# Kernel tuning notes

Measured on AMD Instinct MI355X. Metric: run time of the kernel, lower is better.

## Reference

```python
import jax, jax.numpy as jnp
import numpy as np

PAD_ID = 0


def setup_inputs() -> dict:
    key = jax.random.key(0)
    ks = jax.random.split(key, 14)
    B, S, T = 64, 128, 32
    E = H = 512
    V = 32000
    s = 0.02
    return {
        "trg_tokens": jax.random.randint(ks[0], (B, T), 0, V),
        "src_tokens": jax.random.randint(ks[1], (B, S), 0, V),
        "encoder_out": jax.random.normal(ks[2], (S, B, 2 * H), jnp.float32),
        "hidden": jax.random.normal(ks[3], (B, H), jnp.float32),
        "embed_w": jax.random.normal(ks[4], (V, E), jnp.float32) * s,
        "attn_W": jax.random.normal(ks[5], (H, 2 * H + H), jnp.float32) * s,
        "attn_b": jnp.zeros((H,), jnp.float32),
        "v": jax.random.uniform(ks[6], (H,), jnp.float32),
        "W_ih": jax.random.normal(ks[7], (3 * H, 2 * H + E), jnp.float32) * s,
        "W_hh": jax.random.normal(ks[8], (3 * H, H), jnp.float32) * s,
        "b_ih": jnp.zeros((3 * H,), jnp.float32),
        "b_hh": jnp.zeros((3 * H,), jnp.float32),
        "out_W": jax.random.normal(ks[9], (V, 2 * H + H + E), jnp.float32) * s,
        "out_b": jnp.zeros((V,), jnp.float32),
    }


def reference(trg_tokens, src_tokens, encoder_out, hidden, embed_w, attn_W,
              attn_b, v, W_ih, W_hh, b_ih, b_hh, out_W, out_b):
    # trg_tokens: [B, T], src_tokens: [B, S] (transposed inside, as in torch)
    B, T = trg_tokens.shape
    S = src_tokens.shape[1]
    H = hidden.shape[1]
    V = out_W.shape[0]

    # Embedding with padding_idx -> zero row at PAD_ID
    emb = embed_w.at[PAD_ID].set(0.0)
    mask = (src_tokens != PAD_ID)              # [B, S]
    enc_bt = jnp.transpose(encoder_out, (1, 0, 2))  # [B, S, 2H]
    trg = trg_tokens.T                          # [T, B]

    def step(h, tok):
        x = emb[tok]                            # [B, E]
        # Bahdanau attention
        hrep = jnp.broadcast_to(h[:, None, :], (B, S, H))
        feat = jnp.concatenate([hrep, enc_bt], axis=2)      # [B, S, H+2H]
        energy = jnp.tanh(feat @ attn_W.T + attn_b)          # [B, S, H]
        scores = jnp.einsum('bsd,d->bs', energy, v)          # [B, S]
        scores = jnp.where(mask, scores, -jnp.inf)
        attn = jax.nn.softmax(scores, axis=1)                # [B, S]
        weighted = jnp.einsum('bs,bsd->bd', attn, enc_bt)    # [B, 2H]
        # GRU cell (torch gate order: r, z, n)
        rnn_in = jnp.concatenate([x, weighted], axis=1)      # [B, E+2H]
        gi = rnn_in @ W_ih.T + b_ih                          # [B, 3H]
        gh = h @ W_hh.T + b_hh                               # [B, 3H]
        i_r, i_z, i_n = jnp.split(gi, 3, axis=1)
        h_r, h_z, h_n = jnp.split(gh, 3, axis=1)
        r = jax.nn.sigmoid(i_r + h_r)
        z = jax.nn.sigmoid(i_z + h_z)
        n = jnp.tanh(i_n + r * h_n)
        h_new = (1.0 - z) * n + z * h                        # [B, H]
        # Output projection over cat(output, weighted, x)
        out_feat = jnp.concatenate([h_new, weighted, x], axis=1)  # [B, 2H+H+E]
        logits = out_feat @ out_W.T + out_b                  # [B, V]
        return h_new, logits

    # Teacher forcing ratio = 1.0: inputs are trg[0:T-1]; outputs[0] stays zero
    _, logits_seq = jax.lax.scan(step, hidden, trg[:T - 1])  # [T-1, B, V]
    outputs = jnp.concatenate(
        [jnp.zeros((1, B, V), logits_seq.dtype), logits_seq], axis=0)
    return outputs
```

## Files before the change

kernel.cpp:

```cpp
#include <hip/hip_runtime.h>

typedef __attribute__((ext_vector_type(4))) float f32x4;
typedef __attribute__((ext_vector_type(2))) float f32x2;
typedef __attribute__((ext_vector_type(8))) short s16x8;
typedef __attribute__((ext_vector_type(4))) short s16x4;

#define B_ 64
#define S_ 128
#define T_ 32
#define H_ 512
#define V_ 32000
#define NTILES 2000

#define SY_TILE 32
#define SY_SLOT 64

__device__ __forceinline__ unsigned short f2bf(float f) {
  union { float f; unsigned u; } x; x.f = f;
  unsigned r = x.u + 0x7FFFu + ((x.u >> 16) & 1u);
  return (unsigned short)(r >> 16);
}
__device__ __forceinline__ float bf2f(unsigned short u) {
  union { unsigned u; float f; } x; x.u = ((unsigned)u) << 16; return x.f;
}
__device__ __forceinline__ float fast_tanh(float x) {
  float e = __expf(2.0f * x);
  return 1.0f - 2.0f / (e + 1.0f);
}
__device__ __forceinline__ float fast_sig(float x) {
  return 1.0f / (1.0f + __expf(-x));
}
__device__ __forceinline__ void gload16(const void* g, void* l) {
  __builtin_amdgcn_global_load_lds(
      (const __attribute__((address_space(1))) void*)g,
      (__attribute__((address_space(3))) void*)l, 16, 0, 0);
}
__device__ __forceinline__ void gload16nt(const void* g, void* l) {
  __builtin_amdgcn_global_load_lds(
      (const __attribute__((address_space(1))) void*)g,
      (__attribute__((address_space(3))) void*)l, 16, 0, 2);
}

__device__ __forceinline__ unsigned ald(const unsigned* p) {
  return __hip_atomic_load(p, __ATOMIC_RELAXED, __HIP_MEMORY_SCOPE_AGENT);
}
__device__ __forceinline__ void ast(unsigned* p, unsigned v) {
  __hip_atomic_store(p, v, __ATOMIC_RELAXED, __HIP_MEMORY_SCOPE_AGENT);
}
__device__ __forceinline__ void astf(float* p, float v) {
  union { unsigned u; float f; } x; x.f = v; ast((unsigned*)p, x.u);
}

__device__ __forceinline__ void phase_sync(unsigned* sync, int bid,
                                           unsigned st_ph, int nmask,
                                           unsigned wt_ph) {
  __syncthreads();
  if (threadIdx.x == 0)
    __hip_atomic_store(&sync[SY_SLOT + bid], st_ph, __ATOMIC_RELAXED,
                       __HIP_MEMORY_SCOPE_AGENT);
  if (threadIdx.x < 64) {
    const unsigned* p = &sync[SY_SLOT + (threadIdx.x & nmask)];
    while (ald(p) < wt_ph) __builtin_amdgcn_s_sleep(1);
  }
  __syncthreads();
}

template <int OUTBF>
__global__ __launch_bounds__(256) void big_gemm_k(
    const unsigned short* __restrict__ A, int lda,
    const unsigned short* __restrict__ W, const float* __restrict__ bias,
    void* __restrict__ Cv, int Mv, int N, int K) {
  __shared__ unsigned short As[128 * 32];
  __shared__ unsigned short Bs[128 * 32];
  const int t = threadIdx.x;
  const int wave = t >> 6, lane = t & 63;
  const int m0 = blockIdx.x * 128, n0 = blockIdx.y * 128;
  const int wm = (wave & 1) * 64, wn = (wave >> 1) * 64;
  const int fr = lane & 15, fq = lane >> 4;

  f32x4 acc[4][4];
#pragma unroll
  for (int i = 0; i < 4; ++i)
#pragma unroll
    for (int j = 0; j < 4; ++j) acc[i][j] = (f32x4){0.f, 0.f, 0.f, 0.f};

  const int g = (((lane & 3) ^ ((lane >> 3) & 3))) * 8;
  const size_t a_g0 = (size_t)(m0 + wave * 32 + (lane >> 2)) * lda + g;
  const size_t b_g0 = (size_t)(n0 + wave * 32 + (lane >> 2)) * K + g;
  unsigned short* As_w = As + wave * 1024;
  unsigned short* Bs_w = Bs + wave * 1024;
  const int sl = (fq ^ ((fr >> 1) & 3)) * 8;

  for (int kk = 0; kk < K; kk += 32) {
    gload16(A + a_g0 + kk, As_w);
    gload16(A + a_g0 + (size_t)16 * lda + kk, As_w + 512);
    gload16(W + b_g0 + kk, Bs_w);
    gload16(W + b_g0 + (size_t)16 * K + kk, Bs_w + 512);
    __syncthreads();
    s16x8 af[4], bfr[4];
#pragma unroll
    for (int f = 0; f < 4; ++f) {
      af[f] = *(const s16x8*)(As + (wm + f * 16 + fr) * 32 + sl);
      bfr[f] = *(const s16x8*)(Bs + (wn + f * 16 + fr) * 32 + sl);
    }
#pragma unroll
    for (int fm = 0; fm < 4; ++fm)
#pragma unroll
      for (int fn = 0; fn < 4; ++fn)
        acc[fm][fn] = __builtin_amdgcn_mfma_f32_16x16x32_bf16(af[fm], bfr[fn],
                                                              acc[fm][fn], 0, 0, 0);
    __syncthreads();
  }

#pragma unroll
  for (int fn = 0; fn < 4; ++fn) {
    int col = n0 + wn + fn * 16 + fr;
    float bv = bias[col];
#pragma unroll
    for (int fm = 0; fm < 4; ++fm) {
      int rb = m0 + wm + fm * 16 + fq * 4;
#pragma unroll
      for (int i = 0; i < 4; ++i) {
        int r = rb + i;
        if (r < Mv) {
          if (OUTBF)
            ((unsigned short*)Cv)[(size_t)r * N + col] = f2bf(acc[fm][fn][i] + bv);
          else
            ((float*)Cv)[(size_t)r * N + col] = acc[fm][fn][i] + bv;
        }
      }
    }
  }
}

__global__ __launch_bounds__(512) void fused_k(
    float* __restrict__ h, unsigned short* __restrict__ hbf_step,
    float* __restrict__ hgh_step, const unsigned short* __restrict__ Wcomb,
    const unsigned short* __restrict__ encp_bf,
    const unsigned short* __restrict__ enc_bf, const float* __restrict__ v,
    const int* __restrict__ src_tok, const unsigned short* __restrict__ Ww,
    const unsigned short* __restrict__ gix, const float* __restrict__ b_hh,
    unsigned short* __restrict__ Abf, const unsigned short* __restrict__ outW,
    const float* __restrict__ out_b, float* __restrict__ out,
    unsigned* __restrict__ sync) {
  __shared__ __align__(16) char smem[65536];
  const int t = threadIdx.x;
  const int lane = t & 63, w = t >> 6;
  const int fr = lane & 15, fq = lane >> 4;

  if (blockIdx.x < 64) {
    unsigned short* A0 = (unsigned short*)smem;
    unsigned short* A1 = (unsigned short*)(smem + 9216);
    unsigned short* W0 = (unsigned short*)(smem + 18432);
    unsigned short* W1 = (unsigned short*)(smem + 25344);
    unsigned short* Wp1 = (unsigned short*)(smem + 32256);
    float* gsm = (float*)smem;
    float* sc = (float*)(smem + 12288);
    const int j = blockIdx.x;
    const int ar = t >> 3, ak = (t & 7) * 8;
    const int p1_n0 = j * 32;
    const int rowt_p1 = w & 3, colt_p1 = w >> 2;

#pragma unroll
    for (int c = 0; c < 4; ++c) {
      int id = t * 4 + c;
      int r = id >> 6, cc = id & 63;
      s16x8 wv = *(const s16x8*)(Wcomb + (size_t)(p1_n0 + r) * 512 + cc * 8);
      *(s16x8*)(Wp1 + r * 520 + cc * 8) = wv;
    }

    const int rowt = (w < 4) ? w : (w - 4);
    const int wgate = ar >> 4, wdr = ar & 15;
    const int d0 = j * 16;
    const unsigned short* wwrow =
        Ww + (size_t)(wgate * 512 + d0 + wdr) * 1024 + ak;
    s16x8 pwreg[16];
    if (j < 32 && t < 384) {
#pragma unroll
      for (int p = 0; p < 16; ++p) pwreg[p] = *(const s16x8*)(wwrow + p * 64);
    }
    __syncthreads();

    for (int step = 0; step < 31; ++step) {
      const unsigned short* hbfS = hbf_step + (size_t)step * 64 * 512;
      unsigned short* hbfS1 = hbf_step + (size_t)(step + 1) * 64 * 512;
      float* hghS = hgh_step + (size_t)step * 64 * 2048;
      const unsigned ph = 3u * step;

      {
        s16x8 pa[8];
#pragma unroll
        for (int p = 0; p < 8; ++p)
          pa[p] = *(const s16x8*)(hbfS + ar * 512 + p * 64 + ak);
        *(s16x8*)(A0 + ar * 72 + ak) = pa[0];
        __syncthreads();
        f32x4 acc = {0.f, 0.f, 0.f, 0.f};
#pragma unroll
        for (int it = 0; it < 8; ++it) {
          unsigned short* bufR = (it & 1) ? A1 : A0;
          unsigned short* bufW = (it & 1) ? A0 : A1;
          s16x8 a0 = *(const s16x8*)(bufR + (rowt_p1 * 16 + fr) * 72 + fq * 8);
          s16x8 a1 =
              *(const s16x8*)(bufR + (rowt_p1 * 16 + fr) * 72 + 32 + fq * 8);
          if (it < 7) *(s16x8*)(bufW + ar * 72 + ak) = pa[it + 1];
          s16x8 b0 =
              *(const s16x8*)(Wp1 + (colt_p1 * 16 + fr) * 520 + it * 64 + fq * 8);
          s16x8 b1 = *(const s16x8*)(Wp1 + (colt_p1 * 16 + fr) * 520 + it * 64 +
                                     32 + fq * 8);
          acc = __builtin_amdgcn_mfma_f32_16x16x32_bf16(a0, b0, acc, 0, 0, 0);
          acc = __builtin_amdgcn_mfma_f32_16x16x32_bf16(a1, b1, acc, 0, 0, 0);
          __syncthreads();
        }
        int col = p1_n0 + colt_p1 * 16 + fr;
#pragma unroll
        for (int i = 0; i < 4; ++i)
          astf(&hghS[(rowt_p1 * 16 + fq * 4 + i) * 2048 + col], acc[i]);
      }
      phase_sync(sync, j, ph + 1, 15, ph + 1);

      {
        const int b = j;
        const float* hp = hghS + (size_t)b * 2048;
        float vh[8], hh[8];
        {
          f32x4 v0 = *(const f32x4*)(v + lane * 8);
          f32x4 v1 = *(const f32x4*)(v + lane * 8 + 4);
          f32x4 h0 = *(const f32x4*)(hp + lane * 8);
          f32x4 h1 = *(const f32x4*)(hp + lane * 8 + 4);
#pragma unroll
          for (int q = 0; q < 4; ++q) {
            vh[q] = v0[q]; vh[4 + q] = v1[q];
            hh[q] = h0[q]; hh[4 + q] = h1[q];
          }
        }
        for (int s = w * 16; s < w * 16 + 16; ++s) {
          s16x8 e =
              *(const s16x8*)(encp_bf + (size_t)(b * 128 + s) * 512 + lane * 8);
          float p = 0.f;
#pragma unroll
          for (int q = 0; q < 8; ++q)
            p += vh[q] * fast_tanh(hh[q] + bf2f((unsigned short)e[q]));
          for (int m = 32; m; m >>= 1) p += __shfl_xor(p, m);
          if (lane == 0)
            sc[s] = (src_tok[b * 128 + s] != 0) ? p : -__builtin_inff();
        }
        __syncthreads();
        if (t < 64) {
          float a0 = sc[t], a1 = sc[t + 64];
          float mx = fmaxf(a0, a1);
          for (int m = 32; m; m >>= 1) mx = fmaxf(mx, __shfl_xor(mx, m));
          float e0 = __expf(a0 - mx), e1 = __expf(a1 - mx);
          float ssum = e0 + e1;
          for (int m = 32; m; m >>= 1) ssum += __shfl_xor(ssum, m);
          float inv = 1.0f / ssum;
          sc[t] = e0 * inv;
          sc[t + 64] = e1 * inv;
        }
        __syncthreads();
        const int d = t * 2;
        float w0 = 0.f, w1 = 0.f;
#pragma unroll 16
        for (int s = 0; s < 128; ++s) {
          float a = sc[s];
          unsigned u = *(const unsigned*)(enc_bf + (size_t)(b * 128 + s) * 1024 + d);
          union { unsigned u; float f; } lo, hi;
          lo.u = u << 16; hi.u = u & 0xffff0000u;
          w0 += a * lo.f; w1 += a * hi.f;
        }
        unsigned pk = ((unsigned)f2bf(w1) << 16) | (unsigned)f2bf(w0);
        ast((unsigned*)(Abf + (size_t)(step * 64 + b) * 2048 + 512 + d), pk);
      }
      phase_sync(sync, j, ph + 2, 63, ph + 2);

      if (j < 32) {
        const int r0 = step * 64;
        const unsigned short* abrow = Abf + (size_t)(r0 + ar) * 2048 + 512 + ak;
        s16x8 pa[16];
#pragma unroll
        for (int p = 0; p < 16; ++p) pa[p] = *(const s16x8*)(abrow + p * 64);
        *(s16x8*)(A0 + ar * 72 + ak) = pa[0];
        if (t < 384) *(s16x8*)(W0 + ar * 72 + ak) = pwreg[0];
        __syncthreads();
        f32x4 acc0 = {0.f, 0.f, 0.f, 0.f}, acc1 = {0.f, 0.f, 0.f, 0.f};
#pragma unroll
        for (int it = 0; it < 16; ++it) {
          unsigned short* aR = (it & 1) ? A1 : A0;
          unsigned short* wR = (it & 1) ? W1 : W0;
          unsigned short* aW = (it & 1) ? A0 : A1;
          unsigned short* wW = (it & 1) ? W0 : W1;
          s16x8 a0 = *(const s16x8*)(aR + (rowt * 16 + fr) * 72 + fq * 8);
          s16x8 a1 = *(const s16x8*)(aR + (rowt * 16 + fr) * 72 + 32 + fq * 8);
          if (it < 15) {
            *(s16x8*)(aW + ar * 72 + ak) = pa[it + 1];
            if (t < 384) *(s16x8*)(wW + ar * 72 + ak) = pwreg[it + 1];
          }
          if (w < 4) {
            s16x8 b0 = *(const s16x8*)(wR + fr * 72 + fq * 8);
            s16x8 b1 = *(const s16x8*)(wR + fr * 72 + 32 + fq * 8);
            s16x8 c0 = *(const s16x8*)(wR + (32 + fr) * 72 + fq * 8);
            s16x8 c1 = *(const s16x8*)(wR + (32 + fr) * 72 + 32 + fq * 8);
            acc0 = __builtin_amdgcn_mfma_f32_16x16x32_bf16(a0, b0, acc0, 0, 0, 0);
            acc0 = __builtin_amdgcn_mfma_f32_16x16x32_bf16(a1, b1, acc0, 0, 0, 0);
            acc1 = __builtin_amdgcn_mfma_f32_16x16x32_bf16(a0, c0, acc1, 0, 0, 0);
            acc1 = __builtin_amdgcn_mfma_f32_16x16x32_bf16(a1, c1, acc1, 0, 0, 0);
          } else {
            s16x8 b0 = *(const s16x8*)(wR + (16 + fr) * 72 + fq * 8);
            s16x8 b1 = *(const s16x8*)(wR + (16 + fr) * 72 + 32 + fq * 8);
            acc0 = __builtin_amdgcn_mfma_f32_16x16x32_bf16(a0, b0, acc0, 0, 0, 0);
            acc0 = __builtin_amdgcn_mfma_f32_16x16x32_bf16(a1, b1, acc0, 0, 0, 0);
          }
          __syncthreads();
        }
        {
          const int colt0 = (w < 4) ? 0 : 1;
#pragma unroll
          for (int i = 0; i < 4; ++i) {
            int row = rowt * 16 + fq * 4 + i;
            gsm[row * 48 + colt0 * 16 + fr] =
                acc0[i] +
                bf2f(gix[(size_t)(r0 + row) * 1536 + colt0 * 512 + d0 + fr]);
          }
          if (w < 4) {
#pragma unroll
            for (int i = 0; i < 4; ++i) {
              int row = rowt * 16 + fq * 4 + i;
              gsm[row * 48 + 32 + fr] =
                  acc1[i] + bf2f(gix[(size_t)(r0 + row) * 1536 + 1024 + d0 + fr]);
            }
          }
        }
        __syncthreads();
        {
          int e = t * 2;
          int b = e >> 4, dd = e & 15, d = d0 + dd;
          float hv2[2];
          unsigned short hb2[2];
#pragma unroll
          for (int k = 0; k < 2; ++k) {
            float ir = gsm[b * 48 + dd + k];
            float iz = gsm[b * 48 + 16 + dd + k];
            float inn = gsm[b * 48 + 32 + dd + k];
            float hr = hghS[b * 2048 + 512 + d + k] + b_hh[d + k];
            float hz = hghS[b * 2048 + 1024 + d + k] + b_hh[512 + d + k];
            float hn = hghS[b * 2048 + 1536 + d + k] + b_hh[1024 + d + k];
            float r = fast_sig(ir + hr);
            float z = fast_sig(iz + hz);
            float n = fast_tanh(inn + r * hn);
            hv2[k] = (1.0f - z) * n + z * h[b * 512 + d + k];
            hb2[k] = f2bf(hv2[k]);
          }
          h[b * 512 + d] = hv2[0];
          h[b * 512 + d + 1] = hv2[1];
          unsigned pk = ((unsigned)hb2[1] << 16) | (unsigned)hb2[0];
          ast((unsigned*)(hbfS1 + b * 512 + d), pk);
          ast((unsigned*)(Abf + (size_t)(r0 + b) * 2048 + d), pk);
        }
      }
      phase_sync(sync, j, ph + 3, 31, ph + 3);
    }
  }

  unsigned short* As2 = (unsigned short*)smem;
  unsigned short* Bs2 = (unsigned short*)(smem + 16384);
  unsigned* shp = (unsigned*)(smem + 65532);
  const int wr = (w >> 2) * 64, wc = (w & 3) * 64;

  int rowA[2], cgA[2], rowB[4], cgB[4];
#pragma unroll
  for (int c = 0; c < 2; ++c) {
    int id = (w * 2 + c) * 64 + lane;
    rowA[c] = id >> 3;
    cgA[c] = ((id & 7) - rowA[c]) & 7;
  }
#pragma unroll
  for (int c = 0; c < 4; ++c) {
    int id = (w * 4 + c) * 64 + lane;
    rowB[c] = id >> 3;
    cgB[c] = ((id & 7) - rowB[c]) & 7;
  }

  for (;;) {
    __syncthreads();
    if (t == 0)
      *shp = __hip_atomic_fetch_add(&sync[SY_TILE], 1u, __ATOMIC_RELAXED,
                                    __HIP_MEMORY_SCOPE_AGENT);
    __syncthreads();
    unsigned idx = *shp;
    if (idx >= NTILES) break;
    int mb = idx / 125;
    int nt = idx - mb * 125;
    int gate = mb * 2 + 1;
    if (gate > 30) gate = 30;
    unsigned need = 3u * gate + 3u;
    if (w == 0) {
      const unsigned* p = &sync[SY_SLOT + (lane & 31)];
      while (ald(p) < need) __builtin_amdgcn_s_sleep(16);
    }
    __syncthreads();

    const int m0 = mb * 128, n0 = nt * 256;
    f32x4 acc[4][4];
#pragma unroll
    for (int i = 0; i < 4; ++i)
#pragma unroll
      for (int jj = 0; jj < 4; ++jj) acc[i][jj] = (f32x4){0.f, 0.f, 0.f, 0.f};

    for (int kk = 0; kk < 2048; kk += 64) {
#pragma unroll
      for (int c = 0; c < 2; ++c)
        gload16(Abf + (size_t)(m0 + rowA[c]) * 2048 + kk + cgA[c] * 8,
                As2 + (w * 2 + c) * 512);
#pragma unroll
      for (int c = 0; c < 4; ++c)
        gload16nt(outW + (size_t)(n0 + rowB[c]) * 2048 + kk + cgB[c] * 8,
                  Bs2 + (w * 4 + c) * 512);
      __syncthreads();
#pragma unroll
      for (int kh = 0; kh < 2; ++kh) {
        int cg = kh * 4 + fq;
        s16x8 af[4], bf_[4];
#pragma unroll
        for (int i = 0; i < 4; ++i) {
          int rr = wr + i * 16 + fr;
          af[i] = *(const s16x8*)(As2 + rr * 64 + (((cg + rr) & 7) * 8));
        }
#pragma unroll
        for (int jj = 0; jj < 4; ++jj) {
          int rr = wc + jj * 16 + fr;
          bf_[jj] = *(const s16x8*)(Bs2 + rr * 64 + (((cg + rr) & 7) * 8));
        }
#pragma unroll
        for (int i = 0; i < 4; ++i)
#pragma unroll
          for (int jj = 0; jj < 4; ++jj)
            acc[i][jj] = __builtin_amdgcn_mfma_f32_16x16x32_bf16(
                af[i], bf_[jj], acc[i][jj], 0, 0, 0);
      }
      __syncthreads();
    }

#pragma unroll
    for (int jj = 0; jj < 4; ++jj) {
      int col = n0 + wc + jj * 16 + fr;
      float bv = out_b[col];
#pragma unroll
      for (int i = 0; i < 4; ++i) {
        int rb = m0 + wr + i * 16 + fq * 4;
#pragma unroll
        for (int ii = 0; ii < 4; ++ii) {
          int r = rb + ii;
          if (r < 1984) out[(size_t)(r + 64) * V_ + col] = acc[i][jj][ii] + bv;
        }
      }
    }
  }
}

__global__ __launch_bounds__(256) void cast_bf16_k(const float* __restrict__ src,
                                                   unsigned short* __restrict__ dst,
                                                   int n4) {
  int i = blockIdx.x * 256 + threadIdx.x;
  if (i >= n4) return;
  f32x4 f = *(const f32x4*)(src + (size_t)i * 4);
  s16x4 o;
#pragma unroll
  for (int q = 0; q < 4; ++q) o[q] = (short)f2bf(f[q]);
  *(s16x4*)(dst + (size_t)i * 4) = o;
}

__global__ __launch_bounds__(256) void enc_cast_k(const float* __restrict__ enc,
                                                  unsigned short* __restrict__ dst) {
  int i = blockIdx.x * 256 + threadIdx.x;
  int n = i * 4;
  int row = n >> 10, d = n & 1023;
  int s = row & (S_ - 1), b = row >> 7;
  f32x4 f = *(const f32x4*)(enc + ((size_t)s * B_ + b) * 1024 + d);
  s16x4 o;
#pragma unroll
  for (int q = 0; q < 4; ++q) o[q] = (short)f2bf(f[q]);
  *(s16x4*)(dst + (size_t)row * 1024 + d) = o;
}

__global__ __launch_bounds__(256) void build_wcomb_k(const float* __restrict__ aW,
                                                     const float* __restrict__ whh,
                                                     unsigned short* __restrict__ dst) {
  int idx = (blockIdx.x * 256 + threadIdx.x) * 4;
  int n = idx >> 9, k = idx & 511;
  const float* src = (n < 512) ? (aW + (size_t)n * 1536 + k)
                               : (whh + (size_t)(n - 512) * 512 + k);
  f32x4 f = *(const f32x4*)src;
  s16x4 o;
#pragma unroll
  for (int q = 0; q < 4; ++q) o[q] = (short)f2bf(f[q]);
  *(s16x4*)(dst + idx) = o;
}

__global__ __launch_bounds__(256) void build_wenc_k(const float* __restrict__ aW,
                                                    unsigned short* __restrict__ dst) {
  int idx = (blockIdx.x * 256 + threadIdx.x) * 4;
  int n = idx >> 10, k = idx & 1023;
  f32x4 f = *(const f32x4*)(aW + (size_t)n * 1536 + 512 + k);
  s16x4 o;
#pragma unroll
  for (int q = 0; q < 4; ++q) o[q] = (short)f2bf(f[q]);
  *(s16x4*)(dst + idx) = o;
}

__global__ __launch_bounds__(256) void build_wxw_k(const float* __restrict__ wih,
                                                   unsigned short* __restrict__ wx,
                                                   unsigned short* __restrict__ ww) {
  int flat = blockIdx.x * 256 + threadIdx.x;
  int n = flat / 384, c4 = (flat % 384) * 4;
  f32x4 f = *(const f32x4*)(wih + (size_t)n * 1536 + c4);
  s16x4 o;
#pragma unroll
  for (int q = 0; q < 4; ++q) o[q] = (short)f2bf(f[q]);
  if (c4 < 512)
    *(s16x4*)(wx + (size_t)n * 512 + c4) = o;
  else
    *(s16x4*)(ww + (size_t)n * 1024 + (c4 - 512)) = o;
}

__global__ __launch_bounds__(256) void hcast_k(const float* __restrict__ hidden,
                                               unsigned short* __restrict__ hbf0) {
  int i = blockIdx.x * 256 + threadIdx.x;
  f32x2 f = *(const f32x2*)(hidden + (size_t)i * 2);
  unsigned pk = ((unsigned)f2bf(f[1]) << 16) | (unsigned)f2bf(f[0]);
  *(unsigned*)(hbf0 + (size_t)i * 2) = pk;
}

__global__ __launch_bounds__(256) void xgather_k(const int* __restrict__ trg,
                                                 const float* __restrict__ embed,
                                                 unsigned short* __restrict__ Abf) {
  int row = blockIdx.x;
  int tt = row >> 6, b = row & 63;
  int tok = trg[b * T_ + tt];
  int d = threadIdx.x * 2;
  unsigned pk = 0;
  if (tok != 0) {
    f32x2 f = *(const f32x2*)(embed + (size_t)tok * H_ + d);
    pk = ((unsigned)f2bf(f[1]) << 16) | (unsigned)f2bf(f[0]);
  }
  *(unsigned*)(Abf + (size_t)row * 2048 + 1536 + d) = pk;
}

extern "C" void kernel_launch(void* const* d_in, const int* in_sizes, int n_in,
                              void* d_out, int out_size, void* d_ws, size_t ws_size,
                              hipStream_t stream) {
  const int* trg = (const int*)d_in[0];
  const int* srt = (const int*)d_in[1];
  const float* enc = (const float*)d_in[2];
  const float* hidden = (const float*)d_in[3];
  const float* embed = (const float*)d_in[4];
  const float* attn_W = (const float*)d_in[5];
  const float* attn_b = (const float*)d_in[6];
  const float* vv = (const float*)d_in[7];
  const float* W_ih = (const float*)d_in[8];
  const float* W_hh = (const float*)d_in[9];
  const float* b_ih = (const float*)d_in[10];
  const float* b_hh = (const float*)d_in[11];
  const float* out_W = (const float*)d_in[12];
  const float* out_b = (const float*)d_in[13];
  float* out = (float*)d_out;

  char* ws = (char*)d_ws;
  size_t off = 0;
  auto alloc = [&](size_t bytes) {
    size_t o = off;
    off += (bytes + 255) & ~(size_t)255;
    return ws + o;
  };

  unsigned short* outW_bf = (unsigned short*)alloc((size_t)V_ * 2048 * 2);
  unsigned short* Abf = (unsigned short*)alloc((size_t)2048 * 2048 * 2);
  unsigned short* enc_bf = (unsigned short*)alloc((size_t)B_ * S_ * 1024 * 2);
  unsigned short* encp_bf = (unsigned short*)alloc((size_t)B_ * S_ * 512 * 2);
  unsigned short* gix_bf = (unsigned short*)alloc((size_t)1984 * 1536 * 2);
  unsigned short* Wcomb = (unsigned short*)alloc((size_t)2048 * 512 * 2);
  unsigned short* Wenc = (unsigned short*)alloc((size_t)512 * 1024 * 2);
  unsigned short* Wx = (unsigned short*)alloc((size_t)1536 * 512 * 2);
  unsigned short* Ww = (unsigned short*)alloc((size_t)1536 * 1024 * 2);
  float* hgh_step = (float*)alloc((size_t)31 * B_ * 2048 * 4);
  unsigned short* hbf_step = (unsigned short*)alloc((size_t)32 * B_ * H_ * 2);
  float* h = (float*)alloc((size_t)B_ * H_ * 4);
  unsigned* syncb = (unsigned*)alloc(8192);

  hipMemsetAsync(out, 0, (size_t)B_ * V_ * 4, stream);
  hipMemsetAsync(syncb, 0, 8192, stream);
  hipMemsetAsync(Abf + (size_t)1984 * 2048, 0, (size_t)64 * 2048 * 2, stream);
  hipMemcpyAsync(h, hidden, (size_t)B_ * H_ * 4, hipMemcpyDeviceToDevice, stream);

  cast_bf16_k<<<(V_ * 2048 / 4 + 255) / 256, 256, 0, stream>>>(out_W, outW_bf,
                                                               V_ * 2048 / 4);
  build_wcomb_k<<<2048 * 512 / 4 / 256, 256, 0, stream>>>(attn_W, W_hh, Wcomb);
  build_wenc_k<<<512 * 1024 / 4 / 256, 256, 0, stream>>>(attn_W, Wenc);
  build_wxw_k<<<1536 * 384 / 256, 256, 0, stream>>>(W_ih, Wx, Ww);
  hcast_k<<<64, 256, 0, stream>>>(hidden, hbf_step);
  enc_cast_k<<<B_ * S_ * 1024 / 4 / 256, 256, 0, stream>>>(enc, enc_bf);
  xgather_k<<<1984, 256, 0, stream>>>(trg, embed, Abf);

  big_gemm_k<1><<<dim3(64, 4), 256, 0, stream>>>(enc_bf, 1024, Wenc, attn_b,
                                                 encp_bf, B_ * S_, 512, 1024);
  big_gemm_k<1><<<dim3(16, 12), 256, 0, stream>>>(Abf + 1536, 2048, Wx, b_ih,
                                                  gix_bf, 1984, 1536, 512);

  fused_k<<<256, 512, 0, stream>>>(h, hbf_step, hgh_step, Wcomb, encp_bf, enc_bf,
                                   vv, srt, Ww, gix_bf, b_hh, Abf, outW_bf, out_b,
                                   out, syncb);
}
```

Measured before the change: 1.441 ms.

## Fold hidden-projection phase into attention blocks to remove one grid barrier per step

Each of the 64 attention blocks now computes its own row of the hidden-state attention projection with a local dot product over Wcomb. Blocks 32-63 compute the W_hh gate projections with MFMA, which blocks 0-31 consume after the next barrier. This cuts the per-step grid-wide phase syncs from three to two, shortening the serial recurrence. In exchange every attention block re-reads the 512x512 bf16 projection weight from global memory each step, and the tile-wait thresholds are updated to match the new phase count.

```diff
diff --git a/kernel.cpp b/kernel.cpp
--- a/kernel.cpp
+++ b/kernel.cpp
@@ -153,146 +153,61 @@
     unsigned short* A1 = (unsigned short*)(smem + 9216);
     unsigned short* W0 = (unsigned short*)(smem + 18432);
     unsigned short* W1 = (unsigned short*)(smem + 25344);
-    unsigned short* Wp1 = (unsigned short*)(smem + 32256);
-    float* gsm = (float*)smem;
-    float* sc = (float*)(smem + 12288);
+    float* hpf = (float*)(smem + 32256);
+    float* hpl = (float*)(smem + 34304);
+    float* gsm = (float*)(smem + 36352);
+    float* sc = (float*)(smem + 48640);
     const int j = blockIdx.x;
     const int ar = t >> 3, ak = (t & 7) * 8;
-    const int p1_n0 = j * 32;
-    const int rowt_p1 = w & 3, colt_p1 = w >> 2;
-
-#pragma unroll
-    for (int c = 0; c < 4; ++c) {
-      int id = t * 4 + c;
-      int r = id >> 6, cc = id & 63;
-      s16x8 wv = *(const s16x8*)(Wcomb + (size_t)(p1_n0 + r) * 512 + cc * 8);
-      *(s16x8*)(Wp1 + r * 520 + cc * 8) = wv;
-    }
-
     const int rowt = (w < 4) ? w : (w - 4);
+
+    const int d0 = j * 16;
     const int wgate = ar >> 4, wdr = ar & 15;
-    const int d0 = j * 16;
     const unsigned short* wwrow =
         Ww + (size_t)(wgate * 512 + d0 + wdr) * 1024 + ak;
+    const int wbase = 512 + (j - 32) * 48;
     s16x8 pwreg[16];
-    if (j < 32 && t < 384) {
-#pragma unroll
-      for (int p = 0; p < 16; ++p) pwreg[p] = *(const s16x8*)(wwrow + p * 64);
+    s16x8 wreg1[8];
+    if (j < 32) {
+      if (t < 384) {
+#pragma unroll
+        for (int p = 0; p < 16; ++p) pwreg[p] = *(const s16x8*)(wwrow + p * 64);
+      }
+    } else {
+      if (t < 384) {
+#pragma unroll
+        for (int p = 0; p < 8; ++p)
+          wreg1[p] =
+              *(const s16x8*)(Wcomb + (size_t)(wbase + ar) * 512 + p * 64 + ak);
+      }
     }
-    __syncthreads();
 
     for (int step = 0; step < 31; ++step) {
       const unsigned short* hbfS = hbf_step + (size_t)step * 64 * 512;
       unsigned short* hbfS1 = hbf_step + (size_t)(step + 1) * 64 * 512;
       float* hghS = hgh_step + (size_t)step * 64 * 2048;
-      const unsigned ph = 3u * step;
-
-      {
+      const unsigned ph = 2u * step;
+
+      if (j >= 32) {
         s16x8 pa[8];
 #pragma unroll
         for (int p = 0; p < 8; ++p)
           pa[p] = *(const s16x8*)(hbfS + ar * 512 + p * 64 + ak);
         *(s16x8*)(A0 + ar * 72 + ak) = pa[0];
-        __syncthreads();
-        f32x4 acc = {0.f, 0.f, 0.f, 0.f};
+        if (t < 384) *(s16x8*)(W0 + ar * 72 + ak) = wreg1[0];
+        __syncthreads();
+        f32x4 acc0 = {0.f, 0.f, 0.f, 0.f}, acc1 = {0.f, 0.f, 0.f, 0.f};
 #pragma unroll
         for (int it = 0; it < 8; ++it) {
-          unsigned short* bufR = (it & 1) ? A1 : A0;
-          unsigned short* bufW = (it & 1) ? A0 : A1;
-          s16x8 a0 = *(const s16x8*)(bufR + (rowt_p1 * 16 + fr) * 72 + fq * 8);
-          s16x8 a1 =
-              *(const s16x8*)(bufR + (rowt_p1 * 16 + fr) * 72 + 32 + fq * 8);
-          if (it < 7) *(s16x8*)(bufW + ar * 72 + ak) = pa[it + 1];
-          s16x8 b0 =
-              *(const s16x8*)(Wp1 + (colt_p1 * 16 + fr) * 520 + it * 64 + fq * 8);
-          s16x8 b1 = *(const s16x8*)(Wp1 + (colt_p1 * 16 + fr) * 520 + it * 64 +
-                                     32 + fq * 8);
-          acc = __builtin_amdgcn_mfma_f32_16x16x32_bf16(a0, b0, acc, 0, 0, 0);
-          acc = __builtin_amdgcn_mfma_f32_16x16x32_bf16(a1, b1, acc, 0, 0, 0);
-          __syncthreads();
-        }
-        int col = p1_n0 + colt_p1 * 16 + fr;
-#pragma unroll
-        for (int i = 0; i < 4; ++i)
-          astf(&hghS[(rowt_p1 * 16 + fq * 4 + i) * 2048 + col], acc[i]);
-      }
-      phase_sync(sync, j, ph + 1, 15, ph + 1);
-
-      {
-        const int b = j;
-        const float* hp = hghS + (size_t)b * 2048;
-        float vh[8], hh[8];
-        {
-          f32x4 v0 = *(const f32x4*)(v + lane * 8);
-          f32x4 v1 = *(const f32x4*)(v + lane * 8 + 4);
-          f32x4 h0 = *(const f32x4*)(hp + lane * 8);
-          f32x4 h1 = *(const f32x4*)(hp + lane * 8 + 4);
-#pragma unroll
-          for (int q = 0; q < 4; ++q) {
-            vh[q] = v0[q]; vh[4 + q] = v1[q];
-            hh[q] = h0[q]; hh[4 + q] = h1[q];
-          }
-        }
-        for (int s = w * 16; s < w * 16 + 16; ++s) {
-          s16x8 e =
-              *(const s16x8*)(encp_bf + (size_t)(b * 128 + s) * 512 + lane * 8);
-          float p = 0.f;
-#pragma unroll
-          for (int q = 0; q < 8; ++q)
-            p += vh[q] * fast_tanh(hh[q] + bf2f((unsigned short)e[q]));
-          for (int m = 32; m; m >>= 1) p += __shfl_xor(p, m);
-          if (lane == 0)
-            sc[s] = (src_tok[b * 128 + s] != 0) ? p : -__builtin_inff();
-        }
-        __syncthreads();
-        if (t < 64) {
-          float a0 = sc[t], a1 = sc[t + 64];
-          float mx = fmaxf(a0, a1);
-          for (int m = 32; m; m >>= 1) mx = fmaxf(mx, __shfl_xor(mx, m));
-          float e0 = __expf(a0 - mx), e1 = __expf(a1 - mx);
-          float ssum = e0 + e1;
-          for (int m = 32; m; m >>= 1) ssum += __shfl_xor(ssum, m);
-          float inv = 1.0f / ssum;
-          sc[t] = e0 * inv;
-          sc[t + 64] = e1 * inv;
-        }
-        __syncthreads();
-        const int d = t * 2;
-        float w0 = 0.f, w1 = 0.f;
-#pragma unroll 16
-        for (int s = 0; s < 128; ++s) {
-          float a = sc[s];
-          unsigned u = *(const unsigned*)(enc_bf + (size_t)(b * 128 + s) * 1024 + d);
-          union { unsigned u; float f; } lo, hi;
-          lo.u = u << 16; hi.u = u & 0xffff0000u;
-          w0 += a * lo.f; w1 += a * hi.f;
-        }
-        unsigned pk = ((unsigned)f2bf(w1) << 16) | (unsigned)f2bf(w0);
-        ast((unsigned*)(Abf + (size_t)(step * 64 + b) * 2048 + 512 + d), pk);
-      }
-      phase_sync(sync, j, ph + 2, 63, ph + 2);
-
-      if (j < 32) {
-        const int r0 = step * 64;
-        const unsigned short* abrow = Abf + (size_t)(r0 + ar) * 2048 + 512 + ak;
-        s16x8 pa[16];
-#pragma unroll
-        for (int p = 0; p < 16; ++p) pa[p] = *(const s16x8*)(abrow + p * 64);
-        *(s16x8*)(A0 + ar * 72 + ak) = pa[0];
-        if (t < 384) *(s16x8*)(W0 + ar * 72 + ak) = pwreg[0];
-        __syncthreads();
-        f32x4 acc0 = {0.f, 0.f, 0.f, 0.f}, acc1 = {0.f, 0.f, 0.f, 0.f};
-#pragma unroll
-        for (int it = 0; it < 16; ++it) {
           unsigned short* aR = (it & 1) ? A1 : A0;
           unsigned short* wR = (it & 1) ? W1 : W0;
           unsigned short* aW = (it & 1) ? A0 : A1;
           unsigned short* wW = (it & 1) ? W0 : W1;
           s16x8 a0 = *(const s16x8*)(aR + (rowt * 16 + fr) * 72 + fq * 8);
           s16x8 a1 = *(const s16x8*)(aR + (rowt * 16 + fr) * 72 + 32 + fq * 8);
-          if (it < 15) {
+          if (it < 7) {
             *(s16x8*)(aW + ar * 72 + ak) = pa[it + 1];
-            if (t < 384) *(s16x8*)(wW + ar * 72 + ak) = pwreg[it + 1];
+            if (t < 384) *(s16x8*)(wW + ar * 72 + ak) = wreg1[it + 1];
           }
           if (w < 4) {
             s16x8 b0 = *(const s16x8*)(wR + fr * 72 + fq * 8);
@@ -311,6 +226,138 @@
           }
           __syncthreads();
         }
+        const int colt0 = (w < 4) ? 0 : 1;
+#pragma unroll
+        for (int i = 0; i < 4; ++i) {
+          int row = rowt * 16 + fq * 4 + i;
+          astf(&hghS[(size_t)row * 2048 + wbase + colt0 * 16 + fr], acc0[i]);
+        }
+        if (w < 4) {
+#pragma unroll
+          for (int i = 0; i < 4; ++i) {
+            int row = rowt * 16 + fq * 4 + i;
+            astf(&hghS[(size_t)row * 2048 + wbase + 32 + fr], acc1[i]);
+          }
+        }
+      }
+
+      {
+        const int b = j;
+        __syncthreads();
+        if (t < 64) {
+          s16x8 hb = *(const s16x8*)(hbfS + (size_t)b * 512 + t * 8);
+#pragma unroll
+          for (int q = 0; q < 8; ++q)
+            hpf[t * 8 + q] = bf2f((unsigned short)hb[q]);
+        }
+        __syncthreads();
+        {
+          float acc = 0.f;
+          const unsigned short* wrow = Wcomb + (size_t)t * 512;
+#pragma unroll 8
+          for (int c = 0; c < 64; ++c) {
+            s16x8 w8 = *(const s16x8*)(wrow + c * 8);
+#pragma unroll
+            for (int q = 0; q < 4; ++q) {
+              unsigned uw = ((const unsigned*)&w8)[q];
+              union { unsigned u; float f; } wl, wh;
+              wl.u = uw << 16;
+              wh.u = uw & 0xffff0000u;
+              f32x2 hc = *(const f32x2*)(hpf + c * 8 + 2 * q);
+              acc += wl.f * hc[0] + wh.f * hc[1];
+            }
+          }
+          hpl[t] = acc;
+        }
+        __syncthreads();
+
+        float vh[8], hh[8];
+        {
+          f32x4 v0 = *(const f32x4*)(v + lane * 8);
+          f32x4 v1 = *(const f32x4*)(v + lane * 8 + 4);
+#pragma unroll
+          for (int q = 0; q < 4; ++q) { vh[q] = v0[q]; vh[4 + q] = v1[q]; }
+#pragma unroll
+          for (int q = 0; q < 8; ++q) hh[q] = hpl[lane * 8 + q];
+        }
+        for (int s = w * 16; s < w * 16 + 16; ++s) {
+          s16x8 e =
+              *(const s16x8*)(encp_bf + (size_t)(b * 128 + s) * 512 + lane * 8);
+          float p = 0.f;
+#pragma unroll
+          for (int q = 0; q < 8; ++q)
+            p += vh[q] * fast_tanh(hh[q] + bf2f((unsigned short)e[q]));
+          for (int m = 32; m; m >>= 1) p += __shfl_xor(p, m);
+          if (lane == 0)
+            sc[s] = (src_tok[b * 128 + s] != 0) ? p : -__builtin_inff();
+        }
+        __syncthreads();
+        if (t < 64) {
+          float a0 = sc[t], a1 = sc[t + 64];
+          float mx = fmaxf(a0, a1);
+          for (int m = 32; m; m >>= 1) mx = fmaxf(mx, __shfl_xor(mx, m));
+          float e0 = __expf(a0 - mx), e1 = __expf(a1 - mx);
+          float ssum = e0 + e1;
+          for (int m = 32; m; m >>= 1) ssum += __shfl_xor(ssum, m);
+          float inv = 1.0f / ssum;
+          sc[t] = e0 * inv;
+          sc[t + 64] = e1 * inv;
+        }
+        __syncthreads();
+        const int d = t * 2;
+        float w0 = 0.f, w1 = 0.f;
+#pragma unroll 16
+        for (int s = 0; s < 128; ++s) {
+          float a = sc[s];
+          unsigned u = *(const unsigned*)(enc_bf + (size_t)(b * 128 + s) * 1024 + d);
+          union { unsigned u; float f; } lo, hi;
+          lo.u = u << 16; hi.u = u & 0xffff0000u;
+          w0 += a * lo.f; w1 += a * hi.f;
+        }
+        unsigned pk = ((unsigned)f2bf(w1) << 16) | (unsigned)f2bf(w0);
+        ast((unsigned*)(Abf + (size_t)(step * 64 + b) * 2048 + 512 + d), pk);
+      }
+      phase_sync(sync, j, ph + 1, 63, ph + 1);
+
+      if (j < 32) {
+        const int r0 = step * 64;
+        const unsigned short* abrow = Abf + (size_t)(r0 + ar) * 2048 + 512 + ak;
+        s16x8 pa[16];
+#pragma unroll
+        for (int p = 0; p < 16; ++p) pa[p] = *(const s16x8*)(abrow + p * 64);
+        *(s16x8*)(A0 + ar * 72 + ak) = pa[0];
+        if (t < 384) *(s16x8*)(W0 + ar * 72 + ak) = pwreg[0];
+        __syncthreads();
+        f32x4 acc0 = {0.f, 0.f, 0.f, 0.f}, acc1 = {0.f, 0.f, 0.f, 0.f};
+#pragma unroll
+        for (int it = 0; it < 16; ++it) {
+          unsigned short* aR = (it & 1) ? A1 : A0;
+          unsigned short* wR = (it & 1) ? W1 : W0;
+          unsigned short* aW = (it & 1) ? A0 : A1;
+          unsigned short* wW = (it & 1) ? W0 : W1;
+          s16x8 a0 = *(const s16x8*)(aR + (rowt * 16 + fr) * 72 + fq * 8);
+          s16x8 a1 = *(const s16x8*)(aR + (rowt * 16 + fr) * 72 + 32 + fq * 8);
+          if (it < 15) {
+            *(s16x8*)(aW + ar * 72 + ak) = pa[it + 1];
+            if (t < 384) *(s16x8*)(wW + ar * 72 + ak) = pwreg[it + 1];
+          }
+          if (w < 4) {
+            s16x8 b0 = *(const s16x8*)(wR + fr * 72 + fq * 8);
+            s16x8 b1 = *(const s16x8*)(wR + fr * 72 + 32 + fq * 8);
+            s16x8 c0 = *(const s16x8*)(wR + (32 + fr) * 72 + fq * 8);
+            s16x8 c1 = *(const s16x8*)(wR + (32 + fr) * 72 + 32 + fq * 8);
+            acc0 = __builtin_amdgcn_mfma_f32_16x16x32_bf16(a0, b0, acc0, 0, 0, 0);
+            acc0 = __builtin_amdgcn_mfma_f32_16x16x32_bf16(a1, b1, acc0, 0, 0, 0);
+            acc1 = __builtin_amdgcn_mfma_f32_16x16x32_bf16(a0, c0, acc1, 0, 0, 0);
+            acc1 = __builtin_amdgcn_mfma_f32_16x16x32_bf16(a1, c1, acc1, 0, 0, 0);
+          } else {
+            s16x8 b0 = *(const s16x8*)(wR + (16 + fr) * 72 + fq * 8);
+            s16x8 b1 = *(const s16x8*)(wR + (16 + fr) * 72 + 32 + fq * 8);
+            acc0 = __builtin_amdgcn_mfma_f32_16x16x32_bf16(a0, b0, acc0, 0, 0, 0);
+            acc0 = __builtin_amdgcn_mfma_f32_16x16x32_bf16(a1, b1, acc0, 0, 0, 0);
+          }
+          __syncthreads();
+        }
         {
           const int colt0 = (w < 4) ? 0 : 1;
 #pragma unroll
@@ -356,7 +403,7 @@
           ast((unsigned*)(Abf + (size_t)(r0 + b) * 2048 + d), pk);
         }
       }
-      phase_sync(sync, j, ph + 3, 31, ph + 3);
+      phase_sync(sync, j, ph + 2, 31, ph + 2);
     }
   }
 
@@ -391,7 +438,7 @@
     int nt = idx - mb * 125;
     int gate = mb * 2 + 1;
     if (gate > 30) gate = 30;
-    unsigned need = 3u * gate + 3u;
+    unsigned need = 2u * gate + 2u;
     if (w == 0) {
       const unsigned* p = &sync[SY_SLOT + (lane & 31)];
       while (ald(p) < need) __builtin_amdgcn_s_sleep(16);
```

After: 1.869 ms. 29.8% more time.

## Widen recurrent GEMM K-chunks to 128 and prefetch gate inputs early

Applied to the files above, without the earlier changes.

The per-step recurrent GEMMs in the persistent blocks now stage 128-wide K chunks (row stride 136) instead of 64-wide ones. This halves the number of double-buffered iterations and __syncthreads barriers per step. The phase-1 weight tile is held in registers and streamed through the shared W buffers instead of living as a full resident shared copy. The gix, hgh, bias and old-h loads for the GRU update are issued before the GEMM so their latency overlaps the matrix work, at the cost of more registers.

```diff
diff --git a/kernel.cpp b/kernel.cpp
--- a/kernel.cpp
+++ b/kernel.cpp
@@ -150,36 +150,36 @@
 
   if (blockIdx.x < 64) {
     unsigned short* A0 = (unsigned short*)smem;
-    unsigned short* A1 = (unsigned short*)(smem + 9216);
-    unsigned short* W0 = (unsigned short*)(smem + 18432);
-    unsigned short* W1 = (unsigned short*)(smem + 25344);
-    unsigned short* Wp1 = (unsigned short*)(smem + 32256);
+    unsigned short* A1 = (unsigned short*)(smem + 17408);
+    unsigned short* W0 = (unsigned short*)(smem + 34816);
+    unsigned short* W1 = (unsigned short*)(smem + 47872);
+    float* sc = (float*)(smem + 60928);
     float* gsm = (float*)smem;
-    float* sc = (float*)(smem + 12288);
     const int j = blockIdx.x;
-    const int ar = t >> 3, ak = (t & 7) * 8;
     const int p1_n0 = j * 32;
     const int rowt_p1 = w & 3, colt_p1 = w >> 2;
-
-#pragma unroll
-    for (int c = 0; c < 4; ++c) {
-      int id = t * 4 + c;
-      int r = id >> 6, cc = id & 63;
-      s16x8 wv = *(const s16x8*)(Wcomb + (size_t)(p1_n0 + r) * 512 + cc * 8);
-      *(s16x8*)(Wp1 + r * 520 + cc * 8) = wv;
+    const int rowt = (w < 4) ? w : (w - 4);
+
+    const int a_row = t >> 3, a_c0 = 2 * (t & 7);
+    const int w1_row = t >> 4, w1_c = t & 15;
+    s16x8 wreg1[4];
+#pragma unroll
+    for (int p = 0; p < 4; ++p)
+      wreg1[p] = *(const s16x8*)(Wcomb + (size_t)(p1_n0 + w1_row) * 512 +
+                                 p * 128 + w1_c * 8);
+    const int d0 = j * 16;
+    const int w3_row = t >> 3;
+    const int wg3 = w3_row >> 4, wd3 = w3_row & 15;
+    s16x8 pw[16];
+    if (j < 32 && t < 384) {
+      const unsigned short* wb =
+          Ww + (size_t)(wg3 * 512 + d0 + wd3) * 1024 + a_c0 * 8;
+#pragma unroll
+      for (int p = 0; p < 8; ++p) {
+        pw[2 * p] = *(const s16x8*)(wb + p * 128);
+        pw[2 * p + 1] = *(const s16x8*)(wb + p * 128 + 8);
+      }
     }
-
-    const int rowt = (w < 4) ? w : (w - 4);
-    const int wgate = ar >> 4, wdr = ar & 15;
-    const int d0 = j * 16;
-    const unsigned short* wwrow =
-        Ww + (size_t)(wgate * 512 + d0 + wdr) * 1024 + ak;
-    s16x8 pwreg[16];
-    if (j < 32 && t < 384) {
-#pragma unroll
-      for (int p = 0; p < 16; ++p) pwreg[p] = *(const s16x8*)(wwrow + p * 64);
-    }
-    __syncthreads();
 
     for (int step = 0; step < 31; ++step) {
       const unsigned short* hbfS = hbf_step + (size_t)step * 64 * 512;
@@ -189,26 +189,36 @@
 
       {
         s16x8 pa[8];
-#pragma unroll
-        for (int p = 0; p < 8; ++p)
-          pa[p] = *(const s16x8*)(hbfS + ar * 512 + p * 64 + ak);
-        *(s16x8*)(A0 + ar * 72 + ak) = pa[0];
+        const unsigned short* ab = hbfS + (size_t)a_row * 512 + a_c0 * 8;
+#pragma unroll
+        for (int p = 0; p < 4; ++p) {
+          pa[2 * p] = *(const s16x8*)(ab + p * 128);
+          pa[2 * p + 1] = *(const s16x8*)(ab + p * 128 + 8);
+        }
+        *(s16x8*)(A0 + a_row * 136 + a_c0 * 8) = pa[0];
+        *(s16x8*)(A0 + a_row * 136 + a_c0 * 8 + 8) = pa[1];
+        *(s16x8*)(W0 + w1_row * 136 + w1_c * 8) = wreg1[0];
         __syncthreads();
         f32x4 acc = {0.f, 0.f, 0.f, 0.f};
 #pragma unroll
-        for (int it = 0; it < 8; ++it) {
-          unsigned short* bufR = (it & 1) ? A1 : A0;
-          unsigned short* bufW = (it & 1) ? A0 : A1;
-          s16x8 a0 = *(const s16x8*)(bufR + (rowt_p1 * 16 + fr) * 72 + fq * 8);
-          s16x8 a1 =
-              *(const s16x8*)(bufR + (rowt_p1 * 16 + fr) * 72 + 32 + fq * 8);
-          if (it < 7) *(s16x8*)(bufW + ar * 72 + ak) = pa[it + 1];
-          s16x8 b0 =
-              *(const s16x8*)(Wp1 + (colt_p1 * 16 + fr) * 520 + it * 64 + fq * 8);
-          s16x8 b1 = *(const s16x8*)(Wp1 + (colt_p1 * 16 + fr) * 520 + it * 64 +
-                                     32 + fq * 8);
-          acc = __builtin_amdgcn_mfma_f32_16x16x32_bf16(a0, b0, acc, 0, 0, 0);
-          acc = __builtin_amdgcn_mfma_f32_16x16x32_bf16(a1, b1, acc, 0, 0, 0);
+        for (int it = 0; it < 4; ++it) {
+          unsigned short* aR = (it & 1) ? A1 : A0;
+          unsigned short* wR = (it & 1) ? W1 : W0;
+          unsigned short* aW = (it & 1) ? A0 : A1;
+          unsigned short* wW = (it & 1) ? W0 : W1;
+          if (it < 3) {
+            *(s16x8*)(aW + a_row * 136 + a_c0 * 8) = pa[2 * it + 2];
+            *(s16x8*)(aW + a_row * 136 + a_c0 * 8 + 8) = pa[2 * it + 3];
+            *(s16x8*)(wW + w1_row * 136 + w1_c * 8) = wreg1[it + 1];
+          }
+#pragma unroll
+          for (int sub = 0; sub < 4; ++sub) {
+            s16x8 a =
+                *(const s16x8*)(aR + (rowt_p1 * 16 + fr) * 136 + sub * 32 + fq * 8);
+            s16x8 b =
+                *(const s16x8*)(wR + (colt_p1 * 16 + fr) * 136 + sub * 32 + fq * 8);
+            acc = __builtin_amdgcn_mfma_f32_16x16x32_bf16(a, b, acc, 0, 0, 0);
+          }
           __syncthreads();
         }
         int col = p1_n0 + colt_p1 * 16 + fr;
@@ -274,86 +284,105 @@
 
       if (j < 32) {
         const int r0 = step * 64;
-        const unsigned short* abrow = Abf + (size_t)(r0 + ar) * 2048 + 512 + ak;
+        float gx0[4], gx1[4];
+        const int colt0 = (w < 4) ? 0 : 1;
+#pragma unroll
+        for (int i = 0; i < 4; ++i) {
+          int row = rowt * 16 + fq * 4 + i;
+          gx0[i] = bf2f(gix[(size_t)(r0 + row) * 1536 + colt0 * 512 + d0 + fr]);
+          if (w < 4)
+            gx1[i] = bf2f(gix[(size_t)(r0 + row) * 1536 + 1024 + d0 + fr]);
+        }
+        const int eb = (t * 2) >> 4, ed = (t * 2) & 15, dgl = d0 + ed;
+        float hr2[2], hz2[2], hn2[2], hold[2];
+#pragma unroll
+        for (int k = 0; k < 2; ++k) {
+          hr2[k] = hghS[eb * 2048 + 512 + dgl + k] + b_hh[dgl + k];
+          hz2[k] = hghS[eb * 2048 + 1024 + dgl + k] + b_hh[512 + dgl + k];
+          hn2[k] = hghS[eb * 2048 + 1536 + dgl + k] + b_hh[1024 + dgl + k];
+          hold[k] = h[eb * 512 + dgl + k];
+        }
         s16x8 pa[16];
-#pragma unroll
-        for (int p = 0; p < 16; ++p) pa[p] = *(const s16x8*)(abrow + p * 64);
-        *(s16x8*)(A0 + ar * 72 + ak) = pa[0];
-        if (t < 384) *(s16x8*)(W0 + ar * 72 + ak) = pwreg[0];
+        const unsigned short* ab =
+            Abf + (size_t)(r0 + a_row) * 2048 + 512 + a_c0 * 8;
+#pragma unroll
+        for (int p = 0; p < 8; ++p) {
+          pa[2 * p] = *(const s16x8*)(ab + p * 128);
+          pa[2 * p + 1] = *(const s16x8*)(ab + p * 128 + 8);
+        }
+        *(s16x8*)(A0 + a_row * 136 + a_c0 * 8) = pa[0];
+        *(s16x8*)(A0 + a_row * 136 + a_c0 * 8 + 8) = pa[1];
+        if (t < 384) {
+          *(s16x8*)(W0 + w3_row * 136 + a_c0 * 8) = pw[0];
+          *(s16x8*)(W0 + w3_row * 136 + a_c0 * 8 + 8) = pw[1];
+        }
         __syncthreads();
         f32x4 acc0 = {0.f, 0.f, 0.f, 0.f}, acc1 = {0.f, 0.f, 0.f, 0.f};
 #pragma unroll
-        for (int it = 0; it < 16; ++it) {
+        for (int it = 0; it < 8; ++it) {
           unsigned short* aR = (it & 1) ? A1 : A0;
           unsigned short* wR = (it & 1) ? W1 : W0;
           unsigned short* aW = (it & 1) ? A0 : A1;
           unsigned short* wW = (it & 1) ? W0 : W1;
-          s16x8 a0 = *(const s16x8*)(aR + (rowt * 16 + fr) * 72 + fq * 8);
-          s16x8 a1 = *(const s16x8*)(aR + (rowt * 16 + fr) * 72 + 32 + fq * 8);
-          if (it < 15) {
-            *(s16x8*)(aW + ar * 72 + ak) = pa[it + 1];
-            if (t < 384) *(s16x8*)(wW + ar * 72 + ak) = pwreg[it + 1];
-          }
-          if (w < 4) {
-            s16x8 b0 = *(const s16x8*)(wR + fr * 72 + fq * 8);
-            s16x8 b1 = *(const s16x8*)(wR + fr * 72 + 32 + fq * 8);
-            s16x8 c0 = *(const s16x8*)(wR + (32 + fr) * 72 + fq * 8);
-            s16x8 c1 = *(const s16x8*)(wR + (32 + fr) * 72 + 32 + fq * 8);
-            acc0 = __builtin_amdgcn_mfma_f32_16x16x32_bf16(a0, b0, acc0, 0, 0, 0);
-            acc0 = __builtin_amdgcn_mfma_f32_16x16x32_bf16(a1, b1, acc0, 0, 0, 0);
-            acc1 = __builtin_amdgcn_mfma_f32_16x16x32_bf16(a0, c0, acc1, 0, 0, 0);
-            acc1 = __builtin_amdgcn_mfma_f32_16x16x32_bf16(a1, c1, acc1, 0, 0, 0);
-          } else {
-            s16x8 b0 = *(const s16x8*)(wR + (16 + fr) * 72 + fq * 8);
-            s16x8 b1 = *(const s16x8*)(wR + (16 + fr) * 72 + 32 + fq * 8);
-            acc0 = __builtin_amdgcn_mfma_f32_16x16x32_bf16(a0, b0, acc0, 0, 0, 0);
-            acc0 = __builtin_amdgcn_mfma_f32_16x16x32_bf16(a1, b1, acc0, 0, 0, 0);
+          if (it < 7) {
+            *(s16x8*)(aW + a_row * 136 + a_c0 * 8) = pa[2 * it + 2];
+            *(s16x8*)(aW + a_row * 136 + a_c0 * 8 + 8) = pa[2 * it + 3];
+            if (t < 384) {
+              *(s16x8*)(wW + w3_row * 136 + a_c0 * 8) = pw[2 * it + 2];
+              *(s16x8*)(wW + w3_row * 136 + a_c0 * 8 + 8) = pw[2 * it + 3];
+            }
+          }
+#pragma unroll
+          for (int sub = 0; sub < 4; ++sub) {
+            s16x8 a =
+                *(const s16x8*)(aR + (rowt * 16 + fr) * 136 + sub * 32 + fq * 8);
+            if (w < 4) {
+              s16x8 b = *(const s16x8*)(wR + fr * 136 + sub * 32 + fq * 8);
+              s16x8 c =
+                  *(const s16x8*)(wR + (32 + fr) * 136 + sub * 32 + fq * 8);
+              acc0 = __builtin_amdgcn_mfma_f32_16x16x32_bf16(a, b, acc0, 0, 0, 0);
+              acc1 = __builtin_amdgcn_mfma_f32_16x16x32_bf16(a, c, acc1, 0, 0, 0);
+            } else {
+              s16x8 b = *(const s16x8*)(wR + (16 + fr) * 136 + sub * 32 + fq * 8);
+              acc0 = __builtin_amdgcn_mfma_f32_16x16x32_bf16(a, b, acc0, 0, 0, 0);
+            }
           }
           __syncthreads();
         }
         {
-          const int colt0 = (w < 4) ? 0 : 1;
 #pragma unroll
           for (int i = 0; i < 4; ++i) {
             int row = rowt * 16 + fq * 4 + i;
-            gsm[row * 48 + colt0 * 16 + fr] =
-                acc0[i] +
-                bf2f(gix[(size_t)(r0 + row) * 1536 + colt0 * 512 + d0 + fr]);
+            gsm[row * 48 + colt0 * 16 + fr] = acc0[i] + gx0[i];
           }
           if (w < 4) {
 #pragma unroll
             for (int i = 0; i < 4; ++i) {
               int row = rowt * 16 + fq * 4 + i;
-              gsm[row * 48 + 32 + fr] =
-                  acc1[i] + bf2f(gix[(size_t)(r0 + row) * 1536 + 1024 + d0 + fr]);
+              gsm[row * 48 + 32 + fr] = acc1[i] + gx1[i];
             }
           }
         }
         __syncthreads();
         {
-          int e = t * 2;
-          int b = e >> 4, dd = e & 15, d = d0 + dd;
           float hv2[2];
           unsigned short hb2[2];
 #pragma unroll
           for (int k = 0; k < 2; ++k) {
-            float ir = gsm[b * 48 + dd + k];
-            float iz = gsm[b * 48 + 16 + dd + k];
-            float inn = gsm[b * 48 + 32 + dd + k];
-            float hr = hghS[b * 2048 + 512 + d + k] + b_hh[d + k];
-            float hz = hghS[b * 2048 + 1024 + d + k] + b_hh[512 + d + k];
-            float hn = hghS[b * 2048 + 1536 + d + k] + b_hh[1024 + d + k];
-            float r = fast_sig(ir + hr);
-            float z = fast_sig(iz + hz);
-            float n = fast_tanh(inn + r * hn);
-            hv2[k] = (1.0f - z) * n + z * h[b * 512 + d + k];
+            float ir = gsm[eb * 48 + ed + k];
+            float iz = gsm[eb * 48 + 16 + ed + k];
+            float inn = gsm[eb * 48 + 32 + ed + k];
+            float r = fast_sig(ir + hr2[k]);
+            float z = fast_sig(iz + hz2[k]);
+            float n = fast_tanh(inn + r * hn2[k]);
+            hv2[k] = (1.0f - z) * n + z * hold[k];
             hb2[k] = f2bf(hv2[k]);
           }
-          h[b * 512 + d] = hv2[0];
-          h[b * 512 + d + 1] = hv2[1];
+          h[eb * 512 + dgl] = hv2[0];
+          h[eb * 512 + dgl + 1] = hv2[1];
           unsigned pk = ((unsigned)hb2[1] << 16) | (unsigned)hb2[0];
-          ast((unsigned*)(hbfS1 + b * 512 + d), pk);
-          ast((unsigned*)(Abf + (size_t)(r0 + b) * 2048 + d), pk);
+          ast((unsigned*)(hbfS1 + eb * 512 + dgl), pk);
+          ast((unsigned*)(Abf + (size_t)(r0 + eb) * 2048 + dgl), pk);
         }
       }
       phase_sync(sync, j, ph + 3, 31, ph + 3);
```

Result: slower. 1.479 ms (+2.7%).
